# Kernel optimization log

Hardware: AMD Instinct MI355X
Metric: run time of the kernel (lower is better)

## Reference

```python
import jax, jax.numpy as jnp
import numpy as np

B, L, D, H, NE, M = 4, 1024, 768, 12, 42, 8
OFFSET = 1
NEG = -1e9

def setup_inputs() -> dict:
    key = jax.random.key(0)
    k1, k2, k3, k4 = jax.random.split(key, 4)
    sequence_output = jax.random.normal(k1, (B, L, D), dtype=jnp.float32)
    attention = jax.random.uniform(k2, (B, H, L, L), dtype=jnp.float32)
    mention_idx = jax.random.randint(k3, (B, NE, M), 0, L - 2).astype(jnp.int32)
    mention_mask = jax.random.randint(k4, (B, NE, M), 0, 2).astype(jnp.int32)
    mention_mask = mention_mask.at[:, :, 0].set(1)  # every entity has >=1 mention
    return {"sequence_output": sequence_output, "attention": attention,
            "mention_idx": mention_idx, "mention_mask": mention_mask}

def reference(sequence_output, attention, mention_idx, mention_mask):
    b, l, d = sequence_output.shape
    h = attention.shape[1]
    idx = mention_idx + OFFSET                      # start + offset
    valid = (mention_mask > 0) & (idx < l)          # [B,NE,M], mirrors start+offset < c check
    idx = jnp.where(valid, idx, 0)

    # --- get_hrt: entity embedding = logsumexp over mentions, entity attn = mean over mentions ---
    flat = idx.reshape(b, -1)
    emb = jax.vmap(lambda s, i: s[i])(sequence_output, flat).reshape(b, NE, M, d)
    masked = jnp.where(valid[..., None], emb, NEG)
    ent_emb = jax.nn.logsumexp(masked, axis=2)      # [B,NE,D] (unused downstream, kept faithful)

    att = jax.vmap(lambda a, i: a[:, i])(attention, flat)        # [B,H,NE*M,L]
    att = att.reshape(b, h, NE, M, l)
    vmask = valid.astype(att.dtype)[:, None, :, :, None]         # [B,1,NE,M,1]
    cnt = jnp.maximum(valid.sum(axis=2), 1).astype(att.dtype)    # [B,NE]
    ent_att = (att * vmask).sum(axis=3) / cnt[:, None, :, None]  # [B,H,NE,L]

    # --- get_channel_map: ht_att = mean_h(h_att * t_att), row-normalize, contract with tokens ---
    ht_att = jnp.einsum('bhsl,bhtl->bstl', ent_att, ent_att) / h  # [B,NE,NE,L]
    ht_att = ht_att / (ht_att.sum(axis=-1, keepdims=True) + 1e-5)
    feature_map = jnp.einsum('bstl,bld->bstd', ht_att, sequence_output)  # [B,NE,NE,D]
    return feature_map
```

## Files before the change

kernel.cpp:

```cpp
#include <hip/hip_runtime.h>

#define B_    4
#define L_    1024
#define D_    768
#define H_    12
#define NE_   42
#define M_    8
#define NE2_  (NE_ * NE_)
#define MPAD_ 1792

typedef unsigned short u16;
typedef unsigned int   u32;

__device__ __forceinline__ u16 f2bf(float f) {
    union { float f; u32 u; } c; c.f = f;
    u32 u = c.u;
    u32 r = (u + 0x7FFFu + ((u >> 16) & 1u)) >> 16;
    return (u16)r;
}

__global__ __launch_bounds__(128) void ent_att_kernel(
    const float* __restrict__ att, const int* __restrict__ midx,
    const int* __restrict__ mmask, float* __restrict__ ent) {
    const int h = blockIdx.x, e = blockIdx.y, b = blockIdx.z;
    const int t  = threadIdx.x;
    const int l0 = t * 8;
    const int mb = (b * NE_ + e) * M_;
    const size_t abase = ((size_t)(b * H_ + h)) * L_ * L_;

    float acc[8] = {0.f,0.f,0.f,0.f,0.f,0.f,0.f,0.f};
    int cnt = 0;
    for (int m = 0; m < M_; ++m) {
        int  im = midx[mb + m] + 1;
        bool v  = (mmask[mb + m] > 0) && (im < L_);
        if (v) {
            ++cnt;
            const float* row = att + abase + (size_t)im * L_ + l0;
            float4 x0 = *(const float4*)(row);
            float4 x1 = *(const float4*)(row + 4);
            acc[0] += x0.x; acc[1] += x0.y; acc[2] += x0.z; acc[3] += x0.w;
            acc[4] += x1.x; acc[5] += x1.y; acc[6] += x1.z; acc[7] += x1.w;
        }
    }
    const float s = 1.0f / (float)(cnt < 1 ? 1 : cnt);
    float* o = ent + (((size_t)(b * H_ + h)) * NE_ + e) * L_ + l0;
    *(float4*)(o)     = make_float4(acc[0]*s, acc[1]*s, acc[2]*s, acc[3]*s);
    *(float4*)(o + 4) = make_float4(acc[4]*s, acc[5]*s, acc[6]*s, acc[7]*s);
}

__global__ __launch_bounds__(256) void transpose_kernel(
    const float* __restrict__ S, u16* __restrict__ T) {
    __shared__ u16 tile[32][33];
    const int b  = blockIdx.z;
    const int n0 = blockIdx.x * 32;
    const int k0 = blockIdx.y * 32;
    const int tx = threadIdx.x, ty = threadIdx.y;
    const float* Sb = S + (size_t)b * L_ * D_;
    u16*         Tb = T + (size_t)b * D_ * L_;
    #pragma unroll
    for (int i = 0; i < 4; ++i)
        tile[ty + i*8][tx] = f2bf(Sb[(size_t)(k0 + ty + i*8) * D_ + (n0 + tx)]);
    __syncthreads();
    #pragma unroll
    for (int i = 0; i < 4; ++i)
        Tb[(size_t)(n0 + ty + i*8) * L_ + (k0 + tx)] = tile[tx][ty + i*8];
}

__global__ __launch_bounds__(128) void w_kernel(
    const float* __restrict__ ent, u16* __restrict__ W) {
    const int p = blockIdx.x % MPAD_;
    const int b = blockIdx.x / MPAD_;
    const int t  = threadIdx.x;
    const int l0 = t * 8;
    u16* wrow = W + ((size_t)b * MPAD_ + p) * L_;

    if (p >= NE2_) {
        uint4 z; z.x = z.y = z.z = z.w = 0u;
        *(uint4*)(wrow + l0) = z;
        return;
    }
    const int s  = p / NE_;
    const int tt = p % NE_;
    const float* Eb = ent + (size_t)b * H_ * NE_ * L_;

    float acc[8] = {0.f,0.f,0.f,0.f,0.f,0.f,0.f,0.f};
    for (int h = 0; h < H_; ++h) {
        const float4* as = (const float4*)(Eb + ((size_t)(h * NE_ + s))  * L_ + l0);
        const float4* at = (const float4*)(Eb + ((size_t)(h * NE_ + tt)) * L_ + l0);
        float4 a0 = as[0], a1 = as[1], b0 = at[0], b1 = at[1];
        acc[0] += a0.x * b0.x; acc[1] += a0.y * b0.y;
        acc[2] += a0.z * b0.z; acc[3] += a0.w * b0.w;
        acc[4] += a1.x * b1.x; acc[5] += a1.y * b1.y;
        acc[6] += a1.z * b1.z; acc[7] += a1.w * b1.w;
    }
    float local = acc[0]+acc[1]+acc[2]+acc[3]+acc[4]+acc[5]+acc[6]+acc[7];
    #pragma unroll
    for (int off = 32; off > 0; off >>= 1) local += __shfl_xor(local, off, 64);
    __shared__ float red[2];
    const int wv = t >> 6, ln = t & 63;
    if (ln == 0) red[wv] = local;
    __syncthreads();
    const float tot = red[0] + red[1];
    const float inv = 1.0f / (tot + (float)H_ * 1e-5f);

    u32 w0 = (u32)f2bf(acc[0]*inv) | ((u32)f2bf(acc[1]*inv) << 16);
    u32 w1 = (u32)f2bf(acc[2]*inv) | ((u32)f2bf(acc[3]*inv) << 16);
    u32 w2 = (u32)f2bf(acc[4]*inv) | ((u32)f2bf(acc[5]*inv) << 16);
    u32 w3 = (u32)f2bf(acc[6]*inv) | ((u32)f2bf(acc[7]*inv) << 16);
    uint4 o; o.x = w0; o.y = w1; o.z = w2; o.w = w3;
    *(uint4*)(wrow + l0) = o;
}

typedef __attribute__((ext_vector_type(8))) __bf16 bf16x8;
typedef __attribute__((ext_vector_type(4))) float  f32x4;

__global__ __launch_bounds__(256) void gemm_kernel(
    const u16* __restrict__ W, const u16* __restrict__ T, float* __restrict__ out) {
    __shared__ __align__(16) u16 As[128 * 32];
    __shared__ __align__(16) u16 Bs[128 * 32];
    const int b = blockIdx.z;
    const u16* Ab = W + (size_t)b * MPAD_ * L_ + (size_t)blockIdx.x * 128 * L_;
    const u16* Bb = T + (size_t)b * D_   * L_ + (size_t)blockIdx.y * 128 * L_;
    const int tid  = threadIdx.x;
    const int wave = tid >> 6, lane = tid & 63;
    const int wm = (wave & 1) * 64, wn = (wave >> 1) * 64;
    const int rm = lane & 15, kq = (lane >> 4) * 8;

    f32x4 acc[4][4] = {};

    for (int k0 = 0; k0 < L_; k0 += 32) {
        __syncthreads();
        #pragma unroll
        for (int i = 0; i < 2; ++i) {
            int c = i * 256 + tid;
            int row = c >> 2, ko = (c & 3) * 8;
            __builtin_amdgcn_global_load_lds(
                (const __attribute__((address_space(1))) void*)(Ab + (size_t)row * L_ + k0 + ko),
                (__attribute__((address_space(3))) void*)(&As[c * 8]), 16, 0, 0);
            __builtin_amdgcn_global_load_lds(
                (const __attribute__((address_space(1))) void*)(Bb + (size_t)row * L_ + k0 + ko),
                (__attribute__((address_space(3))) void*)(&Bs[c * 8]), 16, 0, 0);
        }
        __syncthreads();

        bf16x8 af[4], bfr[4];
        #pragma unroll
        for (int i = 0; i < 4; ++i)
            af[i]  = *(const bf16x8*)&As[(wm + i*16 + rm) * 32 + kq];
        #pragma unroll
        for (int j = 0; j < 4; ++j)
            bfr[j] = *(const bf16x8*)&Bs[(wn + j*16 + rm) * 32 + kq];
        #pragma unroll
        for (int i = 0; i < 4; ++i)
            #pragma unroll
            for (int j = 0; j < 4; ++j)
                acc[i][j] = __builtin_amdgcn_mfma_f32_16x16x32_bf16(
                                af[i], bfr[j], acc[i][j], 0, 0, 0);
    }

    const int row0 = blockIdx.x * 128 + wm;
    const int col0 = blockIdx.y * 128 + wn;
    const int cl = lane & 15, rq = (lane >> 4) * 4;
    float* Ob = out + (size_t)b * NE2_ * D_;
    #pragma unroll
    for (int i = 0; i < 4; ++i) {
        #pragma unroll
        for (int j = 0; j < 4; ++j) {
            const int col = col0 + j*16 + cl;
            #pragma unroll
            for (int r = 0; r < 4; ++r) {
                const int row = row0 + i*16 + rq + r;
                if (row < NE2_)
                    Ob[(size_t)row * D_ + col] = acc[i][j][r];
            }
        }
    }
}

#define ENT_BYTES (8257536)
#define W_BYTES   (14680064)

extern "C" void kernel_launch(void* const* d_in, const int* in_sizes, int n_in,
                              void* d_out, int out_size, void* d_ws, size_t ws_size,
                              hipStream_t stream) {
    const float* seq   = (const float*)d_in[0];
    const float* att   = (const float*)d_in[1];
    const int*   midx  = (const int*)d_in[2];
    const int*   mmask = (const int*)d_in[3];
    float* out = (float*)d_out;

    char* ws  = (char*)d_ws;
    float* ent = (float*)ws;
    u16*   W   = (u16*)(ws + ENT_BYTES);
    u16*   ST  = (u16*)(ws + ENT_BYTES + W_BYTES);

    ent_att_kernel<<<dim3(H_, NE_, B_), 128, 0, stream>>>(att, midx, mmask, ent);
    transpose_kernel<<<dim3(D_/32, L_/32, B_), dim3(32, 8), 0, stream>>>(seq, ST);
    w_kernel<<<B_ * MPAD_, 128, 0, stream>>>(ent, W);
    gemm_kernel<<<dim3(MPAD_/128, D_/128, B_), 256, 0, stream>>>(W, ST, out);
}
```

Baseline: 316.4 us.

## Split W construction into a Gram-matrix denominator pass and an LDS-tiled build

Replaces the per-(s,t) w_kernel, which reread both entity-attention rows from global memory for every pair, with two kernels. The first computes the row-sum denominators as a small Gram matrix (sum over h and l of e_s·e_t) using shared-memory tiles and atomicAdd into a buffer that a new kernel zeroes first. The second stages a 16-column chunk of ent for all heads and entities in LDS and writes normalized bf16 W values for every pair. This removes the redundant global reads of ent, at the cost of two extra launches, float atomics that make the summation order nondeterministic, and narrow 8-byte W stores.

```diff
diff --git a/kernel.cpp b/kernel.cpp
--- a/kernel.cpp
+++ b/kernel.cpp
@@ -17,6 +17,11 @@
     u32 u = c.u;
     u32 r = (u + 0x7FFFu + ((u >> 16) & 1u)) >> 16;
     return (u16)r;
+}
+
+__global__ __launch_bounds__(256) void zero_d_kernel(float* __restrict__ D) {
+    int i = blockIdx.x * 256 + threadIdx.x;
+    if (i < B_ * NE2_) D[i] = 0.f;
 }
 
 __global__ __launch_bounds__(128) void ent_att_kernel(
@@ -66,49 +71,98 @@
         Tb[(size_t)(n0 + ty + i*8) * L_ + (k0 + tx)] = tile[tx][ty + i*8];
 }
 
-__global__ __launch_bounds__(128) void w_kernel(
-    const float* __restrict__ ent, u16* __restrict__ W) {
-    const int p = blockIdx.x % MPAD_;
-    const int b = blockIdx.x / MPAD_;
-    const int t  = threadIdx.x;
-    const int l0 = t * 8;
-    u16* wrow = W + ((size_t)b * MPAD_ + p) * L_;
-
-    if (p >= NE2_) {
-        uint4 z; z.x = z.y = z.z = z.w = 0u;
-        *(uint4*)(wrow + l0) = z;
-        return;
-    }
-    const int s  = p / NE_;
-    const int tt = p % NE_;
-    const float* Eb = ent + (size_t)b * H_ * NE_ * L_;
-
-    float acc[8] = {0.f,0.f,0.f,0.f,0.f,0.f,0.f,0.f};
-    for (int h = 0; h < H_; ++h) {
-        const float4* as = (const float4*)(Eb + ((size_t)(h * NE_ + s))  * L_ + l0);
-        const float4* at = (const float4*)(Eb + ((size_t)(h * NE_ + tt)) * L_ + l0);
-        float4 a0 = as[0], a1 = as[1], b0 = at[0], b1 = at[1];
-        acc[0] += a0.x * b0.x; acc[1] += a0.y * b0.y;
-        acc[2] += a0.z * b0.z; acc[3] += a0.w * b0.w;
-        acc[4] += a1.x * b1.x; acc[5] += a1.y * b1.y;
-        acc[6] += a1.z * b1.z; acc[7] += a1.w * b1.w;
-    }
-    float local = acc[0]+acc[1]+acc[2]+acc[3]+acc[4]+acc[5]+acc[6]+acc[7];
-    #pragma unroll
-    for (int off = 32; off > 0; off >>= 1) local += __shfl_xor(local, off, 64);
-    __shared__ float red[2];
-    const int wv = t >> 6, ln = t & 63;
-    if (ln == 0) red[wv] = local;
+#define LQ_    256
+#define PAD3A  260
+
+__global__ __launch_bounds__(256) void denom_kernel(
+    const float* __restrict__ ent, float* __restrict__ D) {
+    __shared__ float es[44 * PAD3A];
+    const int lq = blockIdx.x, h = blockIdx.y, b = blockIdx.z;
+    const int tid = threadIdx.x;
+    const float* Eb = ent + ((size_t)(b * H_ + h) * NE_) * L_ + lq * LQ_;
+
+    for (int i = tid; i < 44 * 64; i += 256) {
+        int r = i >> 6, c = i & 63;
+        float4 v = (r < NE_) ? *(const float4*)(Eb + (size_t)r * L_ + c * 4)
+                             : make_float4(0.f, 0.f, 0.f, 0.f);
+        *(float4*)&es[r * PAD3A + c * 4] = v;
+    }
     __syncthreads();
-    const float tot = red[0] + red[1];
-    const float inv = 1.0f / (tot + (float)H_ * 1e-5f);
-
-    u32 w0 = (u32)f2bf(acc[0]*inv) | ((u32)f2bf(acc[1]*inv) << 16);
-    u32 w1 = (u32)f2bf(acc[2]*inv) | ((u32)f2bf(acc[3]*inv) << 16);
-    u32 w2 = (u32)f2bf(acc[4]*inv) | ((u32)f2bf(acc[5]*inv) << 16);
-    u32 w3 = (u32)f2bf(acc[6]*inv) | ((u32)f2bf(acc[7]*inv) << 16);
-    uint4 o; o.x = w0; o.y = w1; o.z = w2; o.w = w3;
-    *(uint4*)(wrow + l0) = o;
+
+    float* Db = D + b * NE2_;
+    for (int item = tid; item < 242; item += 256) {
+        const int tile = item >> 1, lh = item & 1;
+        const int s0 = (tile / 11) * 4, t0 = (tile % 11) * 4;
+        const float* ps = es + lh * 128;
+        float a[4][4] = {};
+        for (int l4 = 0; l4 < 32; ++l4) {
+            float4 sv[4], tv[4];
+            #pragma unroll
+            for (int j = 0; j < 4; ++j) {
+                sv[j] = *(const float4*)&ps[(s0 + j) * PAD3A + l4 * 4];
+                tv[j] = *(const float4*)&ps[(t0 + j) * PAD3A + l4 * 4];
+            }
+            #pragma unroll
+            for (int j = 0; j < 4; ++j)
+                #pragma unroll
+                for (int k = 0; k < 4; ++k)
+                    a[j][k] += sv[j].x*tv[k].x + sv[j].y*tv[k].y
+                             + sv[j].z*tv[k].z + sv[j].w*tv[k].w;
+        }
+        #pragma unroll
+        for (int j = 0; j < 4; ++j)
+            #pragma unroll
+            for (int k = 0; k < 4; ++k) {
+                int s = s0 + j, t = t0 + k;
+                if (s < NE_ && t < NE_) atomicAdd(Db + s * NE_ + t, a[j][k]);
+            }
+    }
+}
+
+__global__ __launch_bounds__(256) void wbuild_kernel(
+    const float* __restrict__ ent, const float* __restrict__ D,
+    u16* __restrict__ W) {
+    __shared__ float eb[H_ * NE_ * 16];
+    const int lc = blockIdx.x, b = blockIdx.y;
+    const int tid = threadIdx.x;
+    const float* Eb = ent + (size_t)b * H_ * NE_ * L_ + lc * 16;
+
+    for (int i = tid; i < H_ * NE_ * 4; i += 256) {
+        int he = i >> 2, c4 = i & 3;
+        *(float4*)&eb[he * 16 + c4 * 4] = *(const float4*)(Eb + (size_t)he * L_ + c4 * 4);
+    }
+    __syncthreads();
+
+    const int lane = tid & 63, w = tid >> 6;
+    const int lg = lane & 3, tg = lane >> 2;
+    const float* Db = D + b * NE2_;
+    u16* Wb = W + ((size_t)b * MPAD_) * L_ + lc * 16 + lg * 4;
+
+    for (int s = w; s < NE_; s += 4) {
+        float4 es[H_];
+        #pragma unroll
+        for (int h = 0; h < H_; ++h)
+            es[h] = *(const float4*)&eb[(h * NE_ + s) * 16 + lg * 4];
+        for (int t = tg; t < NE_; t += 16) {
+            const float dv = Db[s * NE_ + t];
+            float4 a = {0.f, 0.f, 0.f, 0.f};
+            #pragma unroll
+            for (int h = 0; h < H_; ++h) {
+                float4 e2 = *(const float4*)&eb[(h * NE_ + t) * 16 + lg * 4];
+                a.x += es[h].x * e2.x; a.y += es[h].y * e2.y;
+                a.z += es[h].z * e2.z; a.w += es[h].w * e2.w;
+            }
+            const float inv = 1.0f / (dv + (float)H_ * 1e-5f);
+            ushort4 o;
+            o.x = f2bf(a.x * inv); o.y = f2bf(a.y * inv);
+            o.z = f2bf(a.z * inv); o.w = f2bf(a.w * inv);
+            *(ushort4*)(Wb + (size_t)(s * NE_ + t) * L_) = o;
+        }
+    }
+    for (int i = tid; i < (MPAD_ - NE2_) * 16; i += 256) {
+        int p = NE2_ + (i >> 4), l = i & 15;
+        W[((size_t)b * MPAD_ + p) * L_ + lc * 16 + l] = 0;
+    }
 }
 
 typedef __attribute__((ext_vector_type(8))) __bf16 bf16x8;
@@ -179,6 +233,7 @@
 
 #define ENT_BYTES (8257536)
 #define W_BYTES   (14680064)
+#define ST_BYTES  (6291456)
 
 extern "C" void kernel_launch(void* const* d_in, const int* in_sizes, int n_in,
                               void* d_out, int out_size, void* d_ws, size_t ws_size,
@@ -193,9 +248,12 @@
     float* ent = (float*)ws;
     u16*   W   = (u16*)(ws + ENT_BYTES);
     u16*   ST  = (u16*)(ws + ENT_BYTES + W_BYTES);
-
+    float* Dd  = (float*)(ws + ENT_BYTES + W_BYTES + ST_BYTES);
+
+    zero_d_kernel<<<(B_ * NE2_ + 255) / 256, 256, 0, stream>>>(Dd);
     ent_att_kernel<<<dim3(H_, NE_, B_), 128, 0, stream>>>(att, midx, mmask, ent);
     transpose_kernel<<<dim3(D_/32, L_/32, B_), dim3(32, 8), 0, stream>>>(seq, ST);
-    w_kernel<<<B_ * MPAD_, 128, 0, stream>>>(ent, W);
+    denom_kernel<<<dim3(4, H_, B_), 256, 0, stream>>>(ent, Dd);
+    wbuild_kernel<<<dim3(64, B_), 256, 0, stream>>>(ent, Dd, W);
     gemm_kernel<<<dim3(MPAD_/128, D_/128, B_), 256, 0, stream>>>(W, ST, out);
 }
```

Result: slower. 349.9 us (+10.6%).
